# Performance work log

Hardware: AMD Instinct MI355X
Metric: run time of the kernel (lower is better)

The kernel has to match this reference:

```python
import jax, jax.numpy as jnp
import numpy as np

TOP_K = 2  # cfg.MODEL.MOE.TOP_K


def setup_inputs() -> dict:
    key = jax.random.key(0)
    ks = jax.random.split(key, 5)
    bs, L, d_in, d_out, E = 32, 1024, 768, 256, 8
    return {
        "x": jax.random.normal(ks[0], (bs, L, d_in), dtype=jnp.float32),
        "gate_W": jax.random.normal(ks[1], (d_in, E), dtype=jnp.float32) * (1.0 / np.sqrt(d_in)),
        "gate_b": jax.random.normal(ks[2], (E,), dtype=jnp.float32) * 0.01,
        "expert_W": jax.random.normal(ks[3], (E, d_in, d_out), dtype=jnp.float32) * (1.0 / np.sqrt(d_in)),
        "expert_b": jax.random.normal(ks[4], (E, d_out), dtype=jnp.float32) * 0.01,
    }


def reference(x, gate_W, gate_b, expert_W, expert_b):
    # Gate: (bs, L, E) softmax over experts, then top-k routing weights.
    gate_logits = jnp.einsum("bli,ie->ble", x, gate_W) + gate_b
    gate_weights = jax.nn.softmax(gate_logits, axis=-1)
    topk_vals, topk_idx = jax.lax.top_k(gate_weights, TOP_K)  # (bs, L, K)

    # Dense all-expert projection (E is small), then gather the selected ones.
    # all_out: (bs, L, E, d_out)
    all_out = jnp.einsum("bli,eio->bleo", x, expert_W) + expert_b

    # Select top-k expert outputs per token: (bs, L, K, d_out)
    sel = jnp.take_along_axis(all_out, topk_idx[..., None], axis=2)

    # Weighted combine over the K routed experts -> (bs, L, d_out)
    output = jnp.sum(sel * topk_vals[..., None], axis=2)
    return output
```

## Files before the change

kernel.cpp:

```cpp
#include <hip/hip_runtime.h>
#include <hip/hip_bf16.h>
#include <stdint.h>

#define T_TOKENS 32768
#define D_IN     768
#define D_OUT    256
#define N_EXP    8
#define S_TOT    (T_TOKENS*2)
#define S_PAD    66560
#define NKB      24

typedef __attribute__((ext_vector_type(8))) short bf16x8;
typedef __attribute__((ext_vector_type(4))) float f32x4;

__device__ __forceinline__ unsigned short f2bf(float f) {
    unsigned u = __float_as_uint(f);
    return (unsigned short)((u + 0x7FFFu + ((u >> 16) & 1u)) >> 16);
}
__device__ __forceinline__ unsigned pack_bf2(float a, float b) {
    return (unsigned)f2bf(a) | ((unsigned)f2bf(b) << 16);
}

__device__ __forceinline__ void async16(void* lds, const void* g) {
    __builtin_amdgcn_global_load_lds(
        (const __attribute__((address_space(1))) unsigned int*)g,
        (__attribute__((address_space(3))) unsigned int*)lds, 16, 0, 0);
}

__global__ __launch_bounds__(256) void convw_kernel(
        const float* __restrict__ W, unsigned short* __restrict__ WTb,
        int* __restrict__ zero16) {
    if (blockIdx.x == 0 && threadIdx.x < 16) zero16[threadIdx.x] = 0;
    int eb_ = blockIdx.x;
    int n = threadIdx.x;
    const float* src = W + ((size_t)(eb_ / NKB) * D_IN + (eb_ % NKB) * 32) * 256 + n;
    unsigned pk[16];
    #pragma unroll
    for (int j = 0; j < 16; j++)
        pk[j] = pack_bf2(src[(2*j) * 256], src[(2*j+1) * 256]);
    unsigned* dst = (unsigned*)(WTb + ((size_t)eb_ * 256 + n) * 32);
    #pragma unroll
    for (int j = 0; j < 16; j++) dst[j] = pk[j];
}

__global__ __launch_bounds__(256) void gate_fused_kernel(
        const float* __restrict__ x, const float* __restrict__ gW,
        const float* __restrict__ gb, unsigned short* __restrict__ xbf,
        float* __restrict__ topk_w, int* __restrict__ topk_e,
        int* __restrict__ counts) {
    __shared__ float4 gws4[1536];
    __shared__ int h8[8];
    int tid = threadIdx.x;
    if (tid < 8) h8[tid] = 0;
    #pragma unroll
    for (int i = 0; i < 6; ++i) {
        int f = tid + i * 256;
        gws4[f ^ ((f >> 3) & 7)] = *(const float4*)(gW + f * 4);
    }
    int t0 = blockIdx.x * 32;
    int tt = tid >> 3, qq = tid & 7;
    int t  = t0 + tt;
    const float*    xrow  = x   + (size_t)t * D_IN + qq * 4;
    unsigned short* xbrow = xbf + (size_t)t * D_IN + qq * 4;
    float acc[8] = {0,0,0,0,0,0,0,0};
    __syncthreads();
    #pragma unroll 4
    for (int kk = 0; kk < 24; ++kk) {
        float4 v = *(const float4*)(xrow + kk * 32);
        uint2 p; p.x = pack_bf2(v.x, v.y); p.y = pack_bf2(v.z, v.w);
        *(uint2*)(xbrow + kk * 32) = p;
        float vv[4] = {v.x, v.y, v.z, v.w};
        #pragma unroll
        for (int j = 0; j < 4; ++j) {
            int i0 = 8 * qq + 64 * kk + 2 * j;
            float4 g0 = gws4[i0 ^ qq];
            float4 g1 = gws4[(i0 + 1) ^ qq];
            float xv = vv[j];
            acc[0] += xv * g0.x; acc[1] += xv * g0.y;
            acc[2] += xv * g0.z; acc[3] += xv * g0.w;
            acc[4] += xv * g1.x; acc[5] += xv * g1.y;
            acc[6] += xv * g1.z; acc[7] += xv * g1.w;
        }
    }
    #pragma unroll
    for (int e = 0; e < 8; ++e) {
        acc[e] += __shfl_xor(acc[e], 1);
        acc[e] += __shfl_xor(acc[e], 2);
        acc[e] += __shfl_xor(acc[e], 4);
    }
    if (qq == 0) {
        float mx = -1e30f;
        #pragma unroll
        for (int e = 0; e < 8; ++e) { acc[e] += gb[e]; mx = fmaxf(mx, acc[e]); }
        float w[8], s = 0.f;
        #pragma unroll
        for (int e = 0; e < 8; ++e) { w[e] = expf(acc[e] - mx); s += w[e]; }
        float inv = 1.0f / s;
        int e0 = 0; float b0 = -1.f;
        #pragma unroll
        for (int e = 0; e < 8; ++e) if (w[e] > b0) { b0 = w[e]; e0 = e; }
        int e1 = 0; float b1 = -1.f;
        #pragma unroll
        for (int e = 0; e < 8; ++e) if (e != e0 && w[e] > b1) { b1 = w[e]; e1 = e; }
        topk_w[t*2]   = b0 * inv;
        topk_w[t*2+1] = b1 * inv;
        topk_e[t*2]   = e0;
        topk_e[t*2+1] = e1;
        atomicAdd(&h8[e0], 1); atomicAdd(&h8[e1], 1);
    }
    __syncthreads();
    if (tid < 8) atomicAdd(&counts[tid], h8[tid]);
}

__global__ void scatter_kernel(const int* __restrict__ topk_e, const float* __restrict__ topk_w,
                               const int* __restrict__ counts, int* __restrict__ cursors,
                               int* __restrict__ slot_token, float* __restrict__ slot_w,
                               int* __restrict__ inv_slot) {
    int offs[9]; offs[0] = 0;
    #pragma unroll
    for (int e = 0; e < 8; e++) offs[e+1] = offs[e] + ((counts[e] + 127) & ~127);
    if (blockIdx.x == 0) {
        #pragma unroll
        for (int e = 0; e < 8; e++) {
            int start = offs[e] + counts[e];
            for (int i = start + threadIdx.x; i < offs[e+1]; i += 256) slot_w[i] = 0.f;
        }
    }
    __shared__ int hcnt[8], hbase[8];
    if (threadIdx.x < 8) hcnt[threadIdx.x] = 0;
    __syncthreads();
    int idx[4], ee[4], lr[4];
    int base = blockIdx.x * 256 * 4 + threadIdx.x;
    #pragma unroll
    for (int j = 0; j < 4; j++) {
        idx[j] = base + j * 256;
        ee[j]  = topk_e[idx[j]];
        lr[j]  = atomicAdd(&hcnt[ee[j]], 1);
    }
    __syncthreads();
    if (threadIdx.x < 8) hbase[threadIdx.x] = atomicAdd(&cursors[threadIdx.x], hcnt[threadIdx.x]);
    __syncthreads();
    #pragma unroll
    for (int j = 0; j < 4; j++) {
        int slot = offs[ee[j]] + hbase[ee[j]] + lr[j];
        slot_token[slot] = idx[j] >> 1;
        slot_w[slot]     = topk_w[idx[j]];
        inv_slot[idx[j]] = slot;
    }
}

template<bool ROUTED>
__global__ __launch_bounds__(512, 4) void moe_gemm_kernel(
        const unsigned short* __restrict__ xbf, const unsigned short* __restrict__ WTb,
        const float* __restrict__ eb, const int* __restrict__ counts,
        const int* __restrict__ slot_token, const float* __restrict__ slot_w,
        float* __restrict__ dst) {
    __shared__ unsigned short A_lds[3][128 * 32];

    int lbid = (blockIdx.x & 7) * ((int)gridDim.x >> 3) + (blockIdx.x >> 3);

    int offs[9]; offs[0] = 0;
    #pragma unroll
    for (int e = 0; e < 8; e++) offs[e+1] = offs[e] + ((counts[e] + 127) & ~127);
    int row0 = lbid * 128;
    if (row0 >= offs[8]) return;
    int expert = 0;
    #pragma unroll
    for (int e = 0; e < 8; e++) if (row0 >= offs[e]) expert = e;

    int tid  = threadIdx.x;
    int wave = tid >> 6, lane = tid & 63;
    int lrow = lane & 15, lquad = lane >> 4;
    int wn = wave;

    int ar = tid >> 2, ap = tid & 3;
    int alc = (ap - (ar >> 1)) & 3;
    int tok = slot_token[row0 + ar];
    tok = (tok < 0 || tok >= T_TOKENS) ? 0 : tok;
    const unsigned short* asrc = xbf + (size_t)tok * D_IN + alc * 8;

    const unsigned short* bptr = WTb + (size_t)expert * NKB * 8192
                                     + (wn * 32 + lrow) * 32 + lquad * 8;

    int a_off[8];
    #pragma unroll
    for (int m = 0; m < 8; m++) {
        int r = m * 16 + lrow;
        a_off[m] = r * 32 + ((lquad + (r >> 1)) & 3) * 8;
    }

    f32x4 acc[8][2];
    #pragma unroll
    for (int m = 0; m < 8; m++)
        #pragma unroll
        for (int q = 0; q < 2; q++) acc[m][q] = (f32x4){0,0,0,0};

    bf16x8 bA[2], bB[2];
    auto bload = [&](int kb, bf16x8 (&b)[2]) {
        const unsigned short* bp = bptr + (size_t)kb * 8192;
        #pragma unroll
        for (int q = 0; q < 2; q++) b[q] = *(const bf16x8*)(bp + q * 512);
    };

    int rd = 0, wr = 2;
    auto kstep = [&](int s, bf16x8 (&bcur)[2], bf16x8 (&bnxt)[2]) {
        if (s == NKB - 1) asm volatile("s_waitcnt vmcnt(0)" ::: "memory");
        else              asm volatile("s_waitcnt vmcnt(3)" ::: "memory");
        asm volatile("s_barrier" ::: "memory");
        if (s + 1 < NKB) bload(s + 1, bnxt);
        if (s + 2 < NKB)
            async16(&A_lds[wr][tid * 8], asrc + (s + 2) * 32);
        #pragma unroll
        for (int g = 0; g < 2; ++g) {
            bf16x8 a[4];
            #pragma unroll
            for (int m = 0; m < 4; ++m) a[m] = *(const bf16x8*)&A_lds[rd][a_off[g*4+m]];
            __builtin_amdgcn_s_setprio(1);
            #pragma unroll
            for (int q = 0; q < 2; ++q)
                #pragma unroll
                for (int m = 0; m < 4; ++m)
                    acc[g*4+m][q] = __builtin_amdgcn_mfma_f32_16x16x32_bf16(
                        a[m], bcur[q], acc[g*4+m][q], 0, 0, 0);
            __builtin_amdgcn_s_setprio(0);
        }
        rd = rd == 2 ? 0 : rd + 1;
        wr = wr == 2 ? 0 : wr + 1;
    };

    async16(&A_lds[0][tid * 8], asrc);
    async16(&A_lds[1][tid * 8], asrc + 32);
    __builtin_amdgcn_sched_barrier(0);
    bload(0, bA);
    for (int s = 0; s < NKB; s += 2) {
        kstep(s, bA, bB);
        kstep(s + 1, bB, bA);
    }

    float bias_q[2];
    #pragma unroll
    for (int q = 0; q < 2; q++)
        bias_q[q] = eb[expert * D_OUT + wn * 32 + q * 16 + lrow];
    #pragma unroll
    for (int m = 0; m < 8; m++) {
        #pragma unroll
        for (int r = 0; r < 4; r++) {
            int slot = row0 + m * 16 + lquad * 4 + r;
            if constexpr (ROUTED) {
                float* drow = dst + (size_t)slot * D_OUT + wn * 32;
                #pragma unroll
                for (int q = 0; q < 2; q++)
                    drow[q * 16 + lrow] = acc[m][q][r] + bias_q[q];
            } else {
                int tk = slot_token[slot];
                float wgt = slot_w[slot];
                if (wgt != 0.f) {
                    #pragma unroll
                    for (int q = 0; q < 2; q++)
                        atomicAdd(dst + (size_t)tk * D_OUT + wn * 32 + q * 16 + lrow,
                                  wgt * (acc[m][q][r] + bias_q[q]));
                }
            }
        }
    }
}

__global__ void combine_kernel(const float* __restrict__ routed, const int* __restrict__ inv_slot,
                               const float* __restrict__ topk_w, float* __restrict__ out) {
    int flat = blockIdx.x * 256 + threadIdx.x;
    int t = flat >> 6, c = (flat & 63) * 4;
    int   s0 = inv_slot[t*2], s1 = inv_slot[t*2+1];
    float w0 = topk_w[t*2],   w1 = topk_w[t*2+1];
    float4 r0 = *(const float4*)(routed + (size_t)s0 * D_OUT + c);
    float4 r1 = *(const float4*)(routed + (size_t)s1 * D_OUT + c);
    float4 o;
    o.x = w0*r0.x + w1*r1.x; o.y = w0*r0.y + w1*r1.y;
    o.z = w0*r0.z + w1*r1.z; o.w = w0*r0.w + w1*r1.w;
    *(float4*)(out + (size_t)t * D_OUT + c) = o;
}

extern "C" void kernel_launch(void* const* d_in, const int* in_sizes, int n_in,
                              void* d_out, int out_size, void* d_ws, size_t ws_size,
                              hipStream_t stream) {
    const float* x  = (const float*)d_in[0];
    const float* gW = (const float*)d_in[1];
    const float* gb = (const float*)d_in[2];
    const float* eW = (const float*)d_in[3];
    const float* eb = (const float*)d_in[4];
    float* out = (float*)d_out;
    char* ws = (char*)d_ws;

    float* topk_w      = (float*)(ws + 0);
    int*   topk_e      = (int*)  (ws + 262144);
    int*   counts      = (int*)  (ws + 524288);
    int*   cursors     = (int*)  (ws + 524320);
    int*   slot_token  = (int*)  (ws + 524416);
    float* slot_w      = (float*)(ws + 790656);
    int*   inv_slot    = (int*)  (ws + 1056896);
    unsigned short* WTb= (unsigned short*)(ws + 7610496);
    unsigned short* xbf= (unsigned short*)(ws + 10756224);
    float* routed      = (float*)(ws + 61087872);
    const size_t NEED_ROUTED = 61087872 + (size_t)S_PAD * D_OUT * 4;
    bool use_routed = (ws_size >= NEED_ROUTED);

    convw_kernel      <<<N_EXP * NKB, 256, 0, stream>>>(eW, WTb, counts);
    gate_fused_kernel <<<T_TOKENS / 32, 256, 0, stream>>>(x, gW, gb, xbf,
                                                          topk_w, topk_e, counts);
    scatter_kernel    <<<S_TOT / (256 * 4), 256, 0, stream>>>(topk_e, topk_w, counts, cursors,
                                                              slot_token, slot_w, inv_slot);
    if (use_routed) {
        moe_gemm_kernel<true><<<S_PAD / 128, 512, 0, stream>>>(xbf, WTb, eb, counts,
                                                               slot_token, slot_w, routed);
        combine_kernel<<<T_TOKENS * D_OUT / 4 / 256, 256, 0, stream>>>(routed, inv_slot,
                                                                       topk_w, out);
    } else {
        hipMemsetAsync(slot_token, 0, 532480, stream);
        hipMemsetAsync(out, 0, (size_t)out_size * sizeof(float), stream);
        moe_gemm_kernel<false><<<S_PAD / 128, 512, 0, stream>>>(xbf, WTb, eb, counts,
                                                                slot_token, slot_w, out);
    }
}
```

Measured before the change: 246.5 us.

## Stage two K-blocks of A per barrier to halve pipeline synchronisation

Restructures the GEMM main loop so each iteration stages and consumes two 32-wide K blocks of A in LDS (triple-buffered pairs), halving the number of s_barrier/s_waitcnt sync points. B fragments are loaded from global into registers in an interleaved even/odd pattern. This doubles LDS usage for A (48KB) and changes the vmcnt accounting, which could reduce occupancy or mis-synchronise if the wait counts are wrong.

```diff
diff --git a/kernel.cpp b/kernel.cpp
--- a/kernel.cpp
+++ b/kernel.cpp
@@ -9,6 +9,7 @@
 #define S_TOT    (T_TOKENS*2)
 #define S_PAD    66560
 #define NKB      24
+#define NT2      12
 
 typedef __attribute__((ext_vector_type(8))) short bf16x8;
 typedef __attribute__((ext_vector_type(4))) float f32x4;
@@ -155,7 +156,7 @@
         const float* __restrict__ eb, const int* __restrict__ counts,
         const int* __restrict__ slot_token, const float* __restrict__ slot_w,
         float* __restrict__ dst) {
-    __shared__ unsigned short A_lds[3][128 * 32];
+    __shared__ unsigned short A_lds[3][2][128 * 32];
 
     int lbid = (blockIdx.x & 7) * ((int)gridDim.x >> 3) + (blockIdx.x >> 3);
 
@@ -195,46 +196,50 @@
         #pragma unroll
         for (int q = 0; q < 2; q++) acc[m][q] = (f32x4){0,0,0,0};
 
-    bf16x8 bA[2], bB[2];
     auto bload = [&](int kb, bf16x8 (&b)[2]) {
         const unsigned short* bp = bptr + (size_t)kb * 8192;
         #pragma unroll
         for (int q = 0; q < 2; q++) b[q] = *(const bf16x8*)(bp + q * 512);
     };
-
-    int rd = 0, wr = 2;
-    auto kstep = [&](int s, bf16x8 (&bcur)[2], bf16x8 (&bnxt)[2]) {
-        if (s == NKB - 1) asm volatile("s_waitcnt vmcnt(0)" ::: "memory");
-        else              asm volatile("s_waitcnt vmcnt(3)" ::: "memory");
-        asm volatile("s_barrier" ::: "memory");
-        if (s + 1 < NKB) bload(s + 1, bnxt);
-        if (s + 2 < NKB)
-            async16(&A_lds[wr][tid * 8], asrc + (s + 2) * 32);
+    auto stageA = [&](int st, int t2) {
+        async16(&A_lds[st][0][tid * 8], asrc + (2 * t2) * 32);
+        async16(&A_lds[st][1][tid * 8], asrc + (2 * t2 + 1) * 32);
+    };
+    auto half = [&](const unsigned short* base, bf16x8 (&b)[2]) {
         #pragma unroll
         for (int g = 0; g < 2; ++g) {
             bf16x8 a[4];
             #pragma unroll
-            for (int m = 0; m < 4; ++m) a[m] = *(const bf16x8*)&A_lds[rd][a_off[g*4+m]];
+            for (int m = 0; m < 4; ++m) a[m] = *(const bf16x8*)&base[a_off[g*4+m]];
             __builtin_amdgcn_s_setprio(1);
             #pragma unroll
             for (int q = 0; q < 2; ++q)
                 #pragma unroll
                 for (int m = 0; m < 4; ++m)
                     acc[g*4+m][q] = __builtin_amdgcn_mfma_f32_16x16x32_bf16(
-                        a[m], bcur[q], acc[g*4+m][q], 0, 0, 0);
+                        a[m], b[q], acc[g*4+m][q], 0, 0, 0);
             __builtin_amdgcn_s_setprio(0);
         }
-        rd = rd == 2 ? 0 : rd + 1;
-        wr = wr == 2 ? 0 : wr + 1;
     };
 
-    async16(&A_lds[0][tid * 8], asrc);
-    async16(&A_lds[1][tid * 8], asrc + 32);
+    stageA(0, 0);
+    stageA(1, 1);
     __builtin_amdgcn_sched_barrier(0);
-    bload(0, bA);
-    for (int s = 0; s < NKB; s += 2) {
-        kstep(s, bA, bB);
-        kstep(s + 1, bB, bA);
+    bf16x8 bEv[2];
+    bload(0, bEv);
+
+    for (int t = 0; t < NT2; ++t) {
+        if (t == 0 || t == NT2 - 1) asm volatile("s_waitcnt vmcnt(4)" ::: "memory");
+        else                        asm volatile("s_waitcnt vmcnt(6)" ::: "memory");
+        asm volatile("s_barrier" ::: "memory");
+        bf16x8 bOdd[2];
+        bload(2 * t + 1, bOdd);
+        if (t + 2 < NT2) stageA((t + 2) % 3, t + 2);
+        half(&A_lds[t % 3][0][0], bEv);
+        bf16x8 bEvN[2];
+        if (t + 1 < NT2) bload(2 * t + 2, bEvN);
+        half(&A_lds[t % 3][1][0], bOdd);
+        if (t + 1 < NT2) { bEv[0] = bEvN[0]; bEv[1] = bEvN[1]; }
     }
 
     float bias_q[2];
```

After: 244.4 us. No clear change (-0.9%).
